# Kernel tuning notes

Hardware: AMD Instinct MI355X
Metric: run time of the kernel (lower is better)

Reference implementation:

```python
import jax, jax.numpy as jnp
import numpy as np

NQ = 4
DEPTH = 6
_PAIRS = [(0, 1), (0, 2), (0, 3), (1, 2), (1, 3), (2, 3)]


def _z_signs():
    # sign table (16, 10): columns = [Z0..Z3, Z0Z1, Z0Z2, Z0Z3, Z1Z2, Z1Z3, Z2Z3]
    # wire 0 is the most-significant bit (PennyLane convention)
    bits = (np.arange(16)[:, None] >> np.arange(NQ - 1, -1, -1)[None, :]) & 1
    z = 1.0 - 2.0 * bits  # (16, 4)
    cols = [z[:, i] for i in range(NQ)] + [z[:, i] * z[:, j] for i, j in _PAIRS]
    return np.stack(cols, axis=1).astype(np.float32)  # (16, 10)

_ZSIGNS = jnp.asarray(_z_signs())


def _apply_1q(state, U, q):
    # state: (B, 2,2,2,2); apply 2x2 U on qubit axis 1+q
    s = jnp.moveaxis(state, 1 + q, -1)
    s = jnp.einsum('...j,ij->...i', s, U)
    return jnp.moveaxis(s, -1, 1 + q)


def _cnot(state, c, t):
    a0 = jax.lax.index_in_dim(state, 0, axis=1 + c, keepdims=True)
    a1 = jax.lax.index_in_dim(state, 1, axis=1 + c, keepdims=True)
    a1 = jnp.flip(a1, axis=1 + t)
    return jnp.concatenate([a0, a1], axis=1 + c)


def _circuit(amps, weights):
    # amps: (B, 16) real unit vectors; weights: (DEPTH, NQ)
    B = amps.shape[0]
    psi = amps.astype(jnp.complex64).reshape(B, 2, 2, 2, 2)
    for l in range(DEPTH):
        for q in range(NQ):
            half = weights[l, q] * 0.5
            c = jnp.cos(half).astype(jnp.complex64)
            s = (-1j) * jnp.sin(half).astype(jnp.complex64)
            U = jnp.stack([jnp.stack([c, s]), jnp.stack([s, c])])  # RX gate
            psi = _apply_1q(psi, U, q)
        for q in range(NQ):  # CNOT ring
            psi = _cnot(psi, q, (q + 1) % NQ)
    return psi.reshape(B, 16)


def setup_inputs() -> dict:
    key = jax.random.key(0)
    kx, kw, kh = jax.random.split(key, 3)
    x = jax.random.normal(kx, (8192, 1, 64, 64), dtype=jnp.float32)
    q_weights = jax.random.uniform(kw, (DEPTH, NQ), dtype=jnp.float32, maxval=2.0 * np.pi)
    head_w = jax.random.normal(kh, (10, 10), dtype=jnp.float32) * 0.1
    head_b = jnp.zeros((10,), dtype=jnp.float32)
    scale = jnp.asarray(3.0, dtype=jnp.float32)
    return {"x": x, "q_weights": q_weights, "head_w": head_w, "head_b": head_b, "scale": scale}


def reference(x, q_weights, head_w, head_b, scale):
    B, _, H, W = x.shape
    # adaptive_avg_pool2d to (4,4): average over (H/4, W/4) blocks
    pooled = x.reshape(B, 1, 4, H // 4, 4, W // 4).mean(axis=(3, 5))  # (B,1,4,4)
    v = pooled.reshape(B, 16)
    amps = v / jnp.linalg.norm(v, axis=1, keepdims=True)  # AmplitudeEmbedding(normalize=True)
    psi = _circuit(amps, q_weights)  # (B, 16) complex
    probs = psi.real ** 2 + psi.imag ** 2  # (B, 16)
    feats = probs @ _ZSIGNS  # (B, 10): <Z_i> and <Z_i Z_j>
    out = feats @ head_w.T + head_b
    return out * scale
```

## Files before the change

### kernel.cpp

```cpp
#include <hip/hip_runtime.h>


#define QNET_NQ 4
#define QNET_DEPTH 6

__global__ __launch_bounds__(256) void qnet_tables(
    const float* __restrict__ qw,
    const float* __restrict__ head_w,
    float* __restrict__ tab)
{
    const int t   = threadIdx.x;
    const int k   = t >> 4;
    const int idx = t & 15;

    float re = (idx == k) ? 1.f : 0.f;
    float im = 0.f;
#pragma unroll
    for (int l = 0; l < QNET_DEPTH; ++l) {
#pragma unroll
        for (int q = 0; q < QNET_NQ; ++q) {
            const float half = 0.5f * qw[l * QNET_NQ + q];
            float sn, cs;
            sincosf(half, &sn, &cs);
            const int bit = 1 << (3 - q);
            const float re_p = __shfl_xor(re, bit);
            const float im_p = __shfl_xor(im, bit);
            re = cs * re + sn * im_p;
            im = cs * im - sn * re_p;
        }
#pragma unroll
        for (int q = 0; q < QNET_NQ; ++q) {
            const int cb = 1 << (3 - q);
            const int tb = 1 << (3 - ((q + 1) & 3));
            const float re_s = __shfl_xor(re, tb);
            const float im_s = __shfl_xor(im, tb);
            const bool ctrl = (idx & cb) != 0;
            re = ctrl ? re_s : re;
            im = ctrl ? im_s : im;
        }
    }
    tab[idx * 16 + k]       = re;
    tab[256 + idx * 16 + k] = im;

    if (t < 160) {
        const int r = t >> 4, j = t & 15;
        const float z0 = (j & 8) ? -1.f : 1.f;
        const float z1 = (j & 4) ? -1.f : 1.f;
        const float z2 = (j & 2) ? -1.f : 1.f;
        const float z3 = (j & 1) ? -1.f : 1.f;
        const float* hw = head_w + r * 10;
        tab[512 + t] = z0 * hw[0] + z1 * hw[1] + z2 * hw[2] + z3 * hw[3]
                     + (z0 * z1) * hw[4] + (z0 * z2) * hw[5] + (z0 * z3) * hw[6]
                     + (z1 * z2) * hw[7] + (z1 * z3) * hw[8] + (z2 * z3) * hw[9];
    }
}

__global__ __launch_bounds__(256) void qnet_main(
    const float* __restrict__ x,
    const float* __restrict__ tab,
    const float* __restrict__ head_b,
    const float* __restrict__ scale,
    float* __restrict__ out)
{
    __shared__ float pooled[16];
    __shared__ float ltab[672];

    const int b    = blockIdx.x;
    const int t    = threadIdx.x;
    const int wave = t >> 6;
    const int lane = t & 63;

    for (int i = t; i < 672; i += 256) ltab[i] = tab[i];

    const float* img = x + (size_t)b * 4096 + (size_t)wave * 1024;
    float s = 0.f;
#pragma unroll
    for (int i = 0; i < 4; ++i) {
        float4 v = *reinterpret_cast<const float4*>(img + 4 * (lane + 64 * i));
        s += v.x + v.y + v.z + v.w;
    }
    s += __shfl_xor(s, 32);
    s += __shfl_xor(s, 16);
    s += __shfl_xor(s, 2);
    s += __shfl_xor(s, 1);
    if (lane < 16 && (lane & 3) == 0)
        pooled[wave * 4 + (lane >> 2)] = s * (1.0f / 256.0f);
    __syncthreads();

    if (wave != 0) return;

    const int j = lane & 15;
    float sre = 0.f, sim = 0.f, n2 = 0.f;
#pragma unroll
    for (int k = 0; k < 16; ++k) {
        const float a = pooled[k];
        n2  = fmaf(a, a, n2);
        sre = fmaf(ltab[j * 16 + k], a, sre);
        sim = fmaf(ltab[256 + j * 16 + k], a, sim);
    }
    const float prob = (sre * sre + sim * sim) / n2;

    const int r = (lane < 10) ? lane : 0;
    float acc = 0.f;
#pragma unroll
    for (int jj = 0; jj < 16; ++jj) {
        const float p = __shfl(prob, jj);
        acc = fmaf(ltab[512 + r * 16 + jj], p, acc);
    }
    if (lane < 10)
        out[(size_t)b * 10 + lane] = (head_b[lane] + acc) * scale[0];
}

extern "C" void kernel_launch(void* const* d_in, const int* in_sizes, int n_in,
                              void* d_out, int out_size, void* d_ws, size_t ws_size,
                              hipStream_t stream) {
    const float* x      = (const float*)d_in[0];
    const float* qw     = (const float*)d_in[1];
    const float* head_w = (const float*)d_in[2];
    const float* head_b = (const float*)d_in[3];
    const float* scale  = (const float*)d_in[4];
    float* out = (float*)d_out;
    float* tab = (float*)d_ws;

    const int B = in_sizes[0] / 4096;

    qnet_tables<<<1, 256, 0, stream>>>(qw, head_w, tab);
    qnet_main<<<B, 256, 0, stream>>>(x, tab, head_b, scale, out);
}
```

Measured before the change: 199.1 us.

## Fuse table build into main kernel, one image per wave

Merges the circuit-table kernel into the main kernel, so every block recomputes the 16x16 complex unitary and the head table in shared memory instead of reading it from a workspace. Each block now handles four images, one per wave, with each wave reducing a whole image, and the padded table stride avoids bank conflicts. This removes a kernel launch and the serial dependency between the two kernels, and quarters the block count. The cost is redundant per-block sincos and shuffle work, which may be hidden behind the memory loads since the kernel streams 128 MB.

```diff
diff --git a/kernel.cpp b/kernel.cpp
--- a/kernel.cpp
+++ b/kernel.cpp
@@ -1,114 +1,124 @@
 #include <hip/hip_runtime.h>
 
 
-#define QNET_NQ 4
-#define QNET_DEPTH 6
+#define US 17
+#define TAB_N 714
 
-__global__ __launch_bounds__(256) void qnet_tables(
+__global__ __launch_bounds__(256) void qnet_fused(
+    const float* __restrict__ x,
     const float* __restrict__ qw,
     const float* __restrict__ head_w,
-    float* __restrict__ tab)
+    const float* __restrict__ head_b,
+    const float* __restrict__ scale,
+    float* __restrict__ out,
+    int B)
 {
-    const int t   = threadIdx.x;
-    const int k   = t >> 4;
-    const int idx = t & 15;
+    __shared__ float ltab[TAB_N];
+    __shared__ float pool_s[4][16];
+    __shared__ float prob_s[4][16];
 
-    float re = (idx == k) ? 1.f : 0.f;
-    float im = 0.f;
+    const int t  = threadIdx.x;
+    const int wv = t >> 6;
+    const int ln = t & 63;
+    const int m  = ln & 15;
+
+    const int ib  = blockIdx.x * 4 + wv;
+    const int ibc = (ib < B) ? ib : 0;
+    const float* img = x + (size_t)ibc * 4096;
+
+    float s0 = 0.f, s1 = 0.f, s2 = 0.f, s3 = 0.f;
 #pragma unroll
-    for (int l = 0; l < QNET_DEPTH; ++l) {
+    for (int i = 0; i < 16; ++i) {
+        const float4 u = *reinterpret_cast<const float4*>(img + 4 * ln + 256 * i);
+        const float r = (u.x + u.y) + (u.z + u.w);
+        if (i < 4)       s0 += r;
+        else if (i < 8)  s1 += r;
+        else if (i < 12) s2 += r;
+        else             s3 += r;
+    }
+    s0 += __shfl_xor(s0, 1); s0 += __shfl_xor(s0, 2);
+    s0 += __shfl_xor(s0, 16); s0 += __shfl_xor(s0, 32);
+    s1 += __shfl_xor(s1, 1); s1 += __shfl_xor(s1, 2);
+    s1 += __shfl_xor(s1, 16); s1 += __shfl_xor(s1, 32);
+    s2 += __shfl_xor(s2, 1); s2 += __shfl_xor(s2, 2);
+    s2 += __shfl_xor(s2, 16); s2 += __shfl_xor(s2, 32);
+    s3 += __shfl_xor(s3, 1); s3 += __shfl_xor(s3, 2);
+    s3 += __shfl_xor(s3, 16); s3 += __shfl_xor(s3, 32);
+
+    if (ln < 16 && (ln & 3) == 0) {
+        const int cb = ln >> 2;
+        pool_s[wv][ 0 + cb] = s0 * (1.f / 256.f);
+        pool_s[wv][ 4 + cb] = s1 * (1.f / 256.f);
+        pool_s[wv][ 8 + cb] = s2 * (1.f / 256.f);
+        pool_s[wv][12 + cb] = s3 * (1.f / 256.f);
+    }
+
+    {
+        const int k   = t >> 4;
+        const int idx = t & 15;
+        float re = (idx == k) ? 1.f : 0.f;
+        float im = 0.f;
 #pragma unroll
-        for (int q = 0; q < QNET_NQ; ++q) {
-            const float half = 0.5f * qw[l * QNET_NQ + q];
-            float sn, cs;
-            sincosf(half, &sn, &cs);
-            const int bit = 1 << (3 - q);
-            const float re_p = __shfl_xor(re, bit);
-            const float im_p = __shfl_xor(im, bit);
-            re = cs * re + sn * im_p;
-            im = cs * im - sn * re_p;
+        for (int layer = 0; layer < 6; ++layer) {
+#pragma unroll
+            for (int q = 0; q < 4; ++q) {
+                const float half = 0.5f * qw[layer * 4 + q];
+                float sn, cs;
+                sincosf(half, &sn, &cs);
+                const int bit = 1 << (3 - q);
+                const float re_p = __shfl_xor(re, bit);
+                const float im_p = __shfl_xor(im, bit);
+                re = cs * re + sn * im_p;
+                im = cs * im - sn * re_p;
+            }
+#pragma unroll
+            for (int q = 0; q < 4; ++q) {
+                const int cbit = 1 << (3 - q);
+                const int tbit = 1 << (3 - ((q + 1) & 3));
+                const float re_s = __shfl_xor(re, tbit);
+                const float im_s = __shfl_xor(im, tbit);
+                const bool c1 = (idx & cbit) != 0;
+                re = c1 ? re_s : re;
+                im = c1 ? im_s : im;
+            }
         }
-#pragma unroll
-        for (int q = 0; q < QNET_NQ; ++q) {
-            const int cb = 1 << (3 - q);
-            const int tb = 1 << (3 - ((q + 1) & 3));
-            const float re_s = __shfl_xor(re, tb);
-            const float im_s = __shfl_xor(im, tb);
-            const bool ctrl = (idx & cb) != 0;
-            re = ctrl ? re_s : re;
-            im = ctrl ? im_s : im;
+        ltab[idx * US + k]       = re;
+        ltab[272 + idx * US + k] = im;
+
+        if (t < 160) {
+            const int r = t >> 4, j = t & 15;
+            const float z0 = (j & 8) ? -1.f : 1.f;
+            const float z1 = (j & 4) ? -1.f : 1.f;
+            const float z2 = (j & 2) ? -1.f : 1.f;
+            const float z3 = (j & 1) ? -1.f : 1.f;
+            const float* hw = head_w + r * 10;
+            ltab[544 + r * US + j] =
+                  z0 * hw[0] + z1 * hw[1] + z2 * hw[2] + z3 * hw[3]
+                + (z0 * z1) * hw[4] + (z0 * z2) * hw[5] + (z0 * z3) * hw[6]
+                + (z1 * z2) * hw[7] + (z1 * z3) * hw[8] + (z2 * z3) * hw[9];
         }
     }
-    tab[idx * 16 + k]       = re;
-    tab[256 + idx * 16 + k] = im;
-
-    if (t < 160) {
-        const int r = t >> 4, j = t & 15;
-        const float z0 = (j & 8) ? -1.f : 1.f;
-        const float z1 = (j & 4) ? -1.f : 1.f;
-        const float z2 = (j & 2) ? -1.f : 1.f;
-        const float z3 = (j & 1) ? -1.f : 1.f;
-        const float* hw = head_w + r * 10;
-        tab[512 + t] = z0 * hw[0] + z1 * hw[1] + z2 * hw[2] + z3 * hw[3]
-                     + (z0 * z1) * hw[4] + (z0 * z2) * hw[5] + (z0 * z3) * hw[6]
-                     + (z1 * z2) * hw[7] + (z1 * z3) * hw[8] + (z2 * z3) * hw[9];
-    }
-}
-
-__global__ __launch_bounds__(256) void qnet_main(
-    const float* __restrict__ x,
-    const float* __restrict__ tab,
-    const float* __restrict__ head_b,
-    const float* __restrict__ scale,
-    float* __restrict__ out)
-{
-    __shared__ float pooled[16];
-    __shared__ float ltab[672];
-
-    const int b    = blockIdx.x;
-    const int t    = threadIdx.x;
-    const int wave = t >> 6;
-    const int lane = t & 63;
-
-    for (int i = t; i < 672; i += 256) ltab[i] = tab[i];
-
-    const float* img = x + (size_t)b * 4096 + (size_t)wave * 1024;
-    float s = 0.f;
-#pragma unroll
-    for (int i = 0; i < 4; ++i) {
-        float4 v = *reinterpret_cast<const float4*>(img + 4 * (lane + 64 * i));
-        s += v.x + v.y + v.z + v.w;
-    }
-    s += __shfl_xor(s, 32);
-    s += __shfl_xor(s, 16);
-    s += __shfl_xor(s, 2);
-    s += __shfl_xor(s, 1);
-    if (lane < 16 && (lane & 3) == 0)
-        pooled[wave * 4 + (lane >> 2)] = s * (1.0f / 256.0f);
     __syncthreads();
 
-    if (wave != 0) return;
-
-    const int j = lane & 15;
     float sre = 0.f, sim = 0.f, n2 = 0.f;
 #pragma unroll
     for (int k = 0; k < 16; ++k) {
-        const float a = pooled[k];
+        const float a = pool_s[wv][k];
         n2  = fmaf(a, a, n2);
-        sre = fmaf(ltab[j * 16 + k], a, sre);
-        sim = fmaf(ltab[256 + j * 16 + k], a, sim);
+        sre = fmaf(ltab[m * US + k], a, sre);
+        sim = fmaf(ltab[272 + m * US + k], a, sim);
     }
     const float prob = (sre * sre + sim * sim) / n2;
+    if (ln < 16) prob_s[wv][ln] = prob;
+    __syncthreads();
 
-    const int r = (lane < 10) ? lane : 0;
-    float acc = 0.f;
+    if (ln < 10 && ib < B) {
+        float acc = 0.f;
 #pragma unroll
-    for (int jj = 0; jj < 16; ++jj) {
-        const float p = __shfl(prob, jj);
-        acc = fmaf(ltab[512 + r * 16 + jj], p, acc);
+        for (int j = 0; j < 16; ++j)
+            acc = fmaf(ltab[544 + ln * US + j], prob_s[wv][j], acc);
+        out[(size_t)ib * 10 + ln] = (acc + head_b[ln]) * scale[0];
     }
-    if (lane < 10)
-        out[(size_t)b * 10 + lane] = (head_b[lane] + acc) * scale[0];
 }
 
 extern "C" void kernel_launch(void* const* d_in, const int* in_sizes, int n_in,
@@ -120,10 +130,7 @@
     const float* head_b = (const float*)d_in[3];
     const float* scale  = (const float*)d_in[4];
     float* out = (float*)d_out;
-    float* tab = (float*)d_ws;
 
     const int B = in_sizes[0] / 4096;
-
-    qnet_tables<<<1, 256, 0, stream>>>(qw, head_w, tab);
-    qnet_main<<<B, 256, 0, stream>>>(x, tab, head_b, scale, out);
+    qnet_fused<<<(B + 3) / 4, 256, 0, stream>>>(x, qw, head_w, head_b, scale, out, B);
 }
```

Measured after the change: 200.0 us. No clear change (+0.4%).
